# Kernel optimization log

Measured on AMD Instinct MI355X. Metric: run time of the kernel, lower is better.

## Reference

```python
import jax, jax.numpy as jnp
import numpy as np
import math

N_EMBD = 1024
N_HEAD = 16
BLOCK = 2048
SPARSITY = 0.25
B, T = 2, 2048


def _make_mask_logits(rng):
    # Replicates the patterned init in SparseMixtureAttention.__init__.
    S = BLOCK
    logits = np.empty((N_HEAD, S, S), dtype=np.float32)
    for h in range(N_HEAD):
        if h % 3 == 0:  # banded pattern (bandwidth 16)
            i = np.arange(S)
            band = (np.abs(i[:, None] - i[None, :]) <= 16)
            logits[h] = np.where(band, rng.standard_normal((S, S)) + 2.0,
                                 rng.standard_normal((S, S)) - 2.0)
        elif h % 3 == 1:  # strided pattern: every 4th column
            strided = (np.arange(S)[None, :] % 4 == 0)
            logits[h] = np.where(strided, rng.standard_normal((S, S)) + 2.0,
                                 rng.standard_normal((S, S)) - 2.0)
        else:  # random pattern with given sparsity
            rnd = rng.random((S, S)) < SPARSITY
            logits[h] = np.where(rnd, rng.standard_normal((S, S)) + 2.0,
                                 rng.standard_normal((S, S)) - 2.0)
    # keep the diagonal unmasked so no causal row is fully masked (avoids NaN rows)
    d = np.arange(S)
    logits[:, d, d] = np.abs(logits[:, d, d]) + 2.0
    return logits.astype(np.float32)


def setup_inputs() -> dict:
    key = jax.random.key(0)
    ks = jax.random.split(key, 5)
    rng = np.random.default_rng(0)
    return {
        "x": jax.random.normal(ks[0], (B, T, N_EMBD), dtype=jnp.float32),
        "mask_logits": jnp.asarray(_make_mask_logits(rng)),
        "W_attn": jax.random.normal(ks[1], (3 * N_EMBD, N_EMBD), dtype=jnp.float32) * 0.02,
        "b_attn": jnp.zeros((3 * N_EMBD,), dtype=jnp.float32),
        "W_proj": jax.random.normal(ks[2], (N_EMBD, N_EMBD), dtype=jnp.float32) * 0.02,
        "b_proj": jnp.zeros((N_EMBD,), dtype=jnp.float32),
    }


def reference(x, mask_logits, W_attn, b_attn, W_proj, b_proj):
    Bx, Tx, C = x.shape
    H = mask_logits.shape[0]
    D = C // H
    qkv = x @ W_attn.T + b_attn                       # [B,T,3C]
    q, k, v = jnp.split(qkv, 3, axis=-1)
    q = q.reshape(Bx, Tx, H, D)
    k = k.reshape(Bx, Tx, H, D)
    v = v.reshape(Bx, Tx, H, D)
    att = jnp.einsum('bthd,bshd->bhts', q, k) * (1.0 / math.sqrt(D))  # [B,H,T,T]
    # forward value of the STE mask equals the hard mask (probs - probs.detach() == 0)
    keep = jax.nn.sigmoid(mask_logits[:, :Tx, :Tx]) > 0.5             # [H,T,T]
    causal = jnp.tril(jnp.ones((Tx, Tx), dtype=bool))
    mask = causal[None, :, :] & keep                                  # [H,T,T]
    att = jnp.where(mask[None], att, -jnp.inf)
    att = jax.nn.softmax(att, axis=-1)
    y = jnp.einsum('bhts,bshd->bthd', att, v).reshape(Bx, Tx, C)
    return y @ W_proj.T + b_proj
```

## Files before the change

kernel.cpp:

```cpp
#include <hip/hip_runtime.h>
#include <hip/hip_bf16.h>
#include <stdint.h>

typedef unsigned short u16;
typedef unsigned int u32;
typedef unsigned long long u64;
typedef __attribute__((ext_vector_type(8))) short bf16x8;
typedef __attribute__((ext_vector_type(4))) float f32x4;

#define NB 2
#define NH 16
#define TT 2048
#define DD 64
#define CC 1024

__device__ __forceinline__ u16 bf16bits(float f) {
    __hip_bfloat16 h = __float2bfloat16(f);
    return __builtin_bit_cast(unsigned short, h);
}

__device__ __forceinline__ void gload_lds16(const void* g, void* l) {
    __builtin_amdgcn_global_load_lds(
        (const __attribute__((address_space(1))) void*)g,
        (__attribute__((address_space(3))) void*)l, 16, 0, 0);
}

__global__ __launch_bounds__(256) void cvt_kernel(const float* __restrict__ in,
                                                  u16* __restrict__ out, int n4) {
    int idx = blockIdx.x * blockDim.x + threadIdx.x;
    int stride = gridDim.x * blockDim.x;
    for (int i = idx; i < n4; i += stride) {
        float4 v = reinterpret_cast<const float4*>(in)[i];
        ushort4 o;
        o.x = bf16bits(v.x); o.y = bf16bits(v.y);
        o.z = bf16bits(v.z); o.w = bf16bits(v.w);
        reinterpret_cast<ushort4*>(out)[i] = o;
    }
}

__global__ __launch_bounds__(256) void mask_cvt(const float* __restrict__ ml,
                                                unsigned char* __restrict__ mb) {
    int wid = (blockIdx.x * blockDim.x + threadIdx.x) >> 6;
    int lane = threadIdx.x & 63;
    int nwaves = (gridDim.x * blockDim.x) >> 6;
    for (int row = wid; row < NH * TT; row += nwaves) {
        int i = row & (TT - 1);
        const float* src = ml + (size_t)row * TT;
        unsigned char* dst = mb + (size_t)row * (TT / 8);
        for (int c8 = lane; c8 * 8 <= i; c8 += 64) {
            const float4* p = reinterpret_cast<const float4*>(src + c8 * 8);
            float4 a = p[0];
            float4 b = p[1];
            unsigned v = 0;
            v |= (a.x > 0.f) ? 1u : 0u;
            v |= (a.y > 0.f) ? 2u : 0u;
            v |= (a.z > 0.f) ? 4u : 0u;
            v |= (a.w > 0.f) ? 8u : 0u;
            v |= (b.x > 0.f) ? 16u : 0u;
            v |= (b.y > 0.f) ? 32u : 0u;
            v |= (b.z > 0.f) ? 64u : 0u;
            v |= (b.w > 0.f) ? 128u : 0u;
            dst[c8] = (unsigned char)v;
        }
    }
}

template <int MODE>
__global__ __launch_bounds__(256) void gemm_bt(
    const u16* __restrict__ A, const u16* __restrict__ Bw,
    const float* __restrict__ bias,
    u16* __restrict__ Qb, u16* __restrict__ Kb, u16* __restrict__ Vtb,
    float* __restrict__ Cout, int Kdim) {
    const int bm = blockIdx.y * 128;
    const int bn = blockIdx.x * 128;
    const int tid = threadIdx.x;
    const int w = tid >> 6, lane = tid & 63;
    const int lrow = lane & 15, lgrp = lane >> 4;
    const int wr = (w >> 1) * 64, wc = (w & 1) * 64;

    __shared__ __align__(16) u16 ABs[2][128 * 64];
    u16* As = ABs[0];
    u16* Bs = ABs[1];

    f32x4 acc[4][4] = {};

    const int nkt = Kdim >> 6;
    for (int kt = 0; kt < nkt; ++kt) {
        const int k0 = kt << 6;
#pragma unroll
        for (int i = 0; i < 4; ++i) {
            int e = i * 2048 + tid * 8;
            int r = e >> 6, c = e & 63;
            gload_lds16(A + (size_t)(bm + r) * Kdim + k0 + c, (char*)As + i * 4096 + w * 1024);
            gload_lds16(Bw + (size_t)(bn + r) * Kdim + k0 + c, (char*)Bs + i * 4096 + w * 1024);
        }
        __syncthreads();
#pragma unroll
        for (int kk = 0; kk < 2; ++kk) {
            bf16x8 af[4], bfz[4];
#pragma unroll
            for (int i = 0; i < 4; ++i)
                af[i] = *reinterpret_cast<const bf16x8*>(&As[(wr + i * 16 + lrow) * 64 + kk * 32 + lgrp * 8]);
#pragma unroll
            for (int i = 0; i < 4; ++i)
                bfz[i] = *reinterpret_cast<const bf16x8*>(&Bs[(wc + i * 16 + lrow) * 64 + kk * 32 + lgrp * 8]);
#pragma unroll
            for (int mi = 0; mi < 4; ++mi)
#pragma unroll
                for (int ni = 0; ni < 4; ++ni)
                    acc[mi][ni] = __builtin_amdgcn_mfma_f32_16x16x32_bf16(af[mi], bfz[ni], acc[mi][ni], 0, 0, 0);
        }
        __syncthreads();
    }

    const int sec = (MODE == 0) ? (bn >> 10) : 1;

    if (MODE == 0 && sec == 2) {
        u16* Tl = &ABs[0][0];
#pragma unroll
        for (int ni = 0; ni < 4; ++ni) {
            int nl = wc + ni * 16 + lrow;
            float bv = bias[bn + nl];
#pragma unroll
            for (int mi = 0; mi < 4; ++mi) {
                int ml = wr + mi * 16 + lgrp * 4;
                u64 pk = 0;
#pragma unroll
                for (int j = 0; j < 4; ++j)
                    pk |= (u64)bf16bits(acc[mi][ni][j] + bv) << (16 * j);
                int byte = nl * 256 + ((ml * 2) ^ ((nl & 7) << 4));
                *reinterpret_cast<u64*>((char*)Tl + byte) = pk;
            }
        }
        __syncthreads();
        int r = tid >> 1, half = tid & 1;
        int h = ((bn & 1023) >> 6) + (r >> 6);
        int d = r & 63;
        int b = bm >> 11;
        u16* gdst = Vtb + (((size_t)b * NH + h) * DD + d) * TT + (bm & 2047) + half * 64;
#pragma unroll
        for (int c = 0; c < 8; ++c) {
            uint4 v = *reinterpret_cast<const uint4*>(
                (char*)Tl + r * 256 + ((half * 128 + c * 16) ^ ((r & 7) << 4)));
            *reinterpret_cast<uint4*>(gdst + c * 8) = v;
        }
        return;
    }

#pragma unroll
    for (int ni = 0; ni < 4; ++ni) {
        int n = bn + wc + ni * 16 + lrow;
        float bv = bias[n];
#pragma unroll
        for (int mi = 0; mi < 4; ++mi) {
#pragma unroll
            for (int j = 0; j < 4; ++j) {
                int m = bm + wr + mi * 16 + lgrp * 4 + j;
                float v = acc[mi][ni][j] + bv;
                if (MODE == 1) {
                    Cout[(size_t)m * 1024 + n] = v;
                } else {
                    int h = (n & 1023) >> 6;
                    int d = n & 63;
                    int b = m >> 11;
                    int t = m & 2047;
                    if (sec == 0) {
                        Qb[(((size_t)b * NH + h) * TT + t) * DD + d] =
                            bf16bits(v * (0.125f * 1.4426950408889634f));
                    } else {
                        Kb[(((size_t)b * NH + h) * TT + t) * DD + d] = bf16bits(v);
                    }
                }
            }
        }
    }
}

__global__ __launch_bounds__(256) void attn_kernel(
    const u16* __restrict__ Qb, const u16* __restrict__ Kb,
    const u16* __restrict__ Vtb, const unsigned char* __restrict__ mb,
    u16* __restrict__ att_out) {
    const int slot = blockIdx.x >> 4;
    const int h = blockIdx.x & 15;
    const int b = blockIdx.y;
    const int qt = (slot < 8) ? 31 - slot
                 : (slot < 16) ? slot + 8
                 : (slot < 24) ? 31 - slot
                 : slot - 24;
    const int tid = threadIdx.x;
    const int w = tid >> 6, lane = tid & 63;
    const int lrow = lane & 15, g = lane >> 4;

    __shared__ __align__(16) u16 Ks[2][64 * 64];
    __shared__ __align__(16) u16 Vts[2][64 * 64];
    __shared__ __align__(16) u16 Ps[4][16 * 64];

    const u16* kg_base = &Kb[((size_t)b * NH + h) * TT * DD];
    const u16* vg_base = &Vtb[((size_t)b * NH + h) * DD * TT];

    auto STAGE = [&](int bufi, int kt) {
#pragma unroll
        for (int i = 0; i < 2; ++i) {
            int e = i * 2048 + tid * 8;
            int r = e >> 6, c = e & 63;
            int cs = c ^ ((r & 7) << 3);
            gload_lds16(kg_base + (size_t)kt * 64 * DD + r * DD + cs,
                        (char*)Ks[bufi] + i * 4096 + w * 1024);
            gload_lds16(vg_base + kt * 64 + (size_t)r * TT + cs,
                        (char*)Vts[bufi] + i * 4096 + w * 1024);
        }
    };

    const int qrow_g = qt * 64 + w * 16 + lrow;
    const int rswz = (lrow & 7) << 4;

    bf16x8 qf[2];
#pragma unroll
    for (int kk = 0; kk < 2; ++kk)
        qf[kk] = *reinterpret_cast<const bf16x8*>(
            &Qb[(((size_t)b * NH + h) * TT + qrow_g) * DD + kk * 32 + g * 8]);

    f32x4 oacc[4] = {};
    float l_run = 0.f;

    const unsigned char* mrow_base = mb + ((size_t)h * TT + qrow_g) * (TT / 8);
    char* PsW = (char*)&Ps[w][0];

    STAGE(0, 0);
    __syncthreads();
    int buf = 0;

#pragma unroll 1
    for (int kt = 0; kt <= qt; ++kt) {
        u64 mw = *reinterpret_cast<const u64*>(mrow_base + kt * 8);
        if (kt < qt) STAGE(buf ^ 1, kt + 1);

        f32x4 s[4] = {};
        __builtin_amdgcn_s_setprio(1);
#pragma unroll
        for (int kk = 0; kk < 2; ++kk)
#pragma unroll
            for (int nt = 0; nt < 4; ++nt) {
                bf16x8 kf = *reinterpret_cast<const bf16x8*>(
                    (char*)Ks[buf] + (((nt * 16 + lrow) * 128 + (kk * 32 + g * 8) * 2) ^ rswz));
                s[nt] = __builtin_amdgcn_mfma_f32_16x16x32_bf16(kf, qf[kk], s[nt], 0, 0, 0);
            }
        __builtin_amdgcn_s_setprio(0);

        u64 mws = mw >> (g * 4);
        u32 mlo = (u32)mws, mhi = (u32)(mws >> 32);
        float rs = 0.f;
        if (kt == qt) {
#pragma unroll
            for (int nt = 0; nt < 4; ++nt)
#pragma unroll
                for (int j = 0; j < 4; ++j) {
                    int bi = nt * 16 + j;
                    bool keep = (((bi < 32 ? mlo : mhi) >> (bi & 31)) & 1) &&
                                (kt * 64 + nt * 16 + g * 4 + j <= qrow_g);
                    float p = keep ? exp2f(s[nt][j]) : 0.f;
                    rs += p;
                    s[nt][j] = p;
                }
        } else {
#pragma unroll
            for (int nt = 0; nt < 4; ++nt)
#pragma unroll
                for (int j = 0; j < 4; ++j) {
                    int bi = nt * 16 + j;
                    bool keep = ((bi < 32 ? mlo : mhi) >> (bi & 31)) & 1;
                    float p = keep ? exp2f(s[nt][j]) : 0.f;
                    rs += p;
                    s[nt][j] = p;
                }
        }
        rs += __shfl_xor(rs, 16);
        rs += __shfl_xor(rs, 32);
        l_run += rs;

#pragma unroll
        for (int nt = 0; nt < 4; ++nt)
#pragma unroll
            for (int t = 0; t < 2; ++t) {
                u32 pk = (u32)bf16bits(s[nt][2 * t]) |
                         ((u32)bf16bits(s[nt][2 * t + 1]) << 16);
                int byte = (lrow * 128 + (nt * 16 + g * 4 + 2 * t) * 2) ^ rswz;
                *reinterpret_cast<u32*>(PsW + byte) = pk;
            }

        __builtin_amdgcn_s_setprio(1);
#pragma unroll
        for (int kk = 0; kk < 2; ++kk) {
            bf16x8 pf = *reinterpret_cast<const bf16x8*>(
                PsW + ((lrow * 128 + (kk * 32 + g * 8) * 2) ^ rswz));
#pragma unroll
            for (int dt = 0; dt < 4; ++dt) {
                bf16x8 vf = *reinterpret_cast<const bf16x8*>(
                    (char*)Vts[buf] + (((dt * 16 + lrow) * 128 + (kk * 32 + g * 8) * 2) ^ rswz));
                oacc[dt] = __builtin_amdgcn_mfma_f32_16x16x32_bf16(pf, vf, oacc[dt], 0, 0, 0);
            }
        }
        __builtin_amdgcn_s_setprio(0);

        __syncthreads();
        buf ^= 1;
    }

    float lb[4];
#pragma unroll
    for (int j = 0; j < 4; ++j)
        lb[j] = __shfl(l_run, (lane & 48) + g * 4 + j);
#pragma unroll
    for (int dt = 0; dt < 4; ++dt)
#pragma unroll
        for (int j = 0; j < 4; ++j) {
            int t = qt * 64 + w * 16 + g * 4 + j;
            float o = oacc[dt][j] / lb[j];
            att_out[((size_t)b * TT + t) * CC + h * DD + dt * 16 + lrow] = bf16bits(o);
        }
}

extern "C" void kernel_launch(void* const* d_in, const int* in_sizes, int n_in,
                              void* d_out, int out_size, void* d_ws, size_t ws_size,
                              hipStream_t stream) {
    const float* x = (const float*)d_in[0];
    const float* mask_logits = (const float*)d_in[1];
    const float* W_attn = (const float*)d_in[2];
    const float* b_attn = (const float*)d_in[3];
    const float* W_proj = (const float*)d_in[4];
    const float* b_proj = (const float*)d_in[5];
    float* out = (float*)d_out;

    char* ws = (char*)d_ws;
    u16* xb  = (u16*)(ws + 0);
    u16* Wa  = (u16*)(ws + (8u << 20));
    u16* Wp  = (u16*)(ws + (14u << 20));
    u16* Qb  = (u16*)(ws + (16u << 20));
    u16* Kb  = (u16*)(ws + (24u << 20));
    u16* Vtb = (u16*)(ws + (32u << 20));
    u16* att = (u16*)(ws + (40u << 20));
    unsigned char* mbits = (unsigned char*)(ws + 0);

    cvt_kernel<<<2048, 256, 0, stream>>>(x, xb, NB * TT * CC / 4);
    cvt_kernel<<<2048, 256, 0, stream>>>(W_attn, Wa, 3 * CC * CC / 4);
    cvt_kernel<<<1024, 256, 0, stream>>>(W_proj, Wp, CC * CC / 4);

    gemm_bt<0><<<dim3(24, 32), 256, 0, stream>>>(xb, Wa, b_attn, Qb, Kb, Vtb, nullptr, CC);
    mask_cvt<<<1024, 256, 0, stream>>>(mask_logits, mbits);
    attn_kernel<<<dim3(512, 2), 256, 0, stream>>>(Qb, Kb, Vtb, mbits, att);
    gemm_bt<1><<<dim3(8, 32), 256, 0, stream>>>(att, Wp, b_proj, nullptr, nullptr, nullptr, out, CC);
}
```

Measured before the change: 176.4 us.

## Fuse mask bit-packing into QKV GEMM and process two query tiles per attention block

```diff
diff --git a/kernel.cpp b/kernel.cpp
--- a/kernel.cpp
+++ b/kernel.cpp
@@ -38,42 +38,44 @@
     }
 }
 
-__global__ __launch_bounds__(256) void mask_cvt(const float* __restrict__ ml,
-                                                unsigned char* __restrict__ mb) {
-    int wid = (blockIdx.x * blockDim.x + threadIdx.x) >> 6;
-    int lane = threadIdx.x & 63;
-    int nwaves = (gridDim.x * blockDim.x) >> 6;
-    for (int row = wid; row < NH * TT; row += nwaves) {
-        int i = row & (TT - 1);
-        const float* src = ml + (size_t)row * TT;
-        unsigned char* dst = mb + (size_t)row * (TT / 8);
-        for (int c8 = lane; c8 * 8 <= i; c8 += 64) {
-            const float4* p = reinterpret_cast<const float4*>(src + c8 * 8);
-            float4 a = p[0];
-            float4 b = p[1];
-            unsigned v = 0;
-            v |= (a.x > 0.f) ? 1u : 0u;
-            v |= (a.y > 0.f) ? 2u : 0u;
-            v |= (a.z > 0.f) ? 4u : 0u;
-            v |= (a.w > 0.f) ? 8u : 0u;
-            v |= (b.x > 0.f) ? 16u : 0u;
-            v |= (b.y > 0.f) ? 32u : 0u;
-            v |= (b.z > 0.f) ? 64u : 0u;
-            v |= (b.w > 0.f) ? 128u : 0u;
-            dst[c8] = (unsigned char)v;
-        }
-    }
-}
-
 template <int MODE>
 __global__ __launch_bounds__(256) void gemm_bt(
     const u16* __restrict__ A, const u16* __restrict__ Bw,
     const float* __restrict__ bias,
     u16* __restrict__ Qb, u16* __restrict__ Kb, u16* __restrict__ Vtb,
-    float* __restrict__ Cout, int Kdim) {
+    float* __restrict__ Cout, const float* __restrict__ ml,
+    unsigned char* __restrict__ mbout, int Kdim) {
+    const int tid = threadIdx.x;
+
+    if (MODE == 0 && blockIdx.x >= 24) {
+        int wid = (blockIdx.y * 8 + (blockIdx.x - 24)) * 4 + (tid >> 6);
+        int lane = tid & 63;
+#pragma unroll 1
+        for (int row = wid; row < NH * TT; row += 1024) {
+            int i = row & (TT - 1);
+            const float* src = ml + (size_t)row * TT;
+            unsigned char* dst = mbout + (size_t)row * (TT / 8);
+            for (int c8 = lane; c8 * 8 <= i; c8 += 64) {
+                const float4* p = reinterpret_cast<const float4*>(src + c8 * 8);
+                float4 a = p[0];
+                float4 bb = p[1];
+                unsigned v = 0;
+                v |= (a.x > 0.f) ? 1u : 0u;
+                v |= (a.y > 0.f) ? 2u : 0u;
+                v |= (a.z > 0.f) ? 4u : 0u;
+                v |= (a.w > 0.f) ? 8u : 0u;
+                v |= (bb.x > 0.f) ? 16u : 0u;
+                v |= (bb.y > 0.f) ? 32u : 0u;
+                v |= (bb.z > 0.f) ? 64u : 0u;
+                v |= (bb.w > 0.f) ? 128u : 0u;
+                dst[c8] = (unsigned char)v;
+            }
+        }
+        return;
+    }
+
     const int bm = blockIdx.y * 128;
     const int bn = blockIdx.x * 128;
-    const int tid = threadIdx.x;
     const int w = tid >> 6, lane = tid & 63;
     const int lrow = lane & 15, lgrp = lane >> 4;
     const int wr = (w >> 1) * 64, wc = (w & 1) * 64;
@@ -123,12 +125,12 @@
             float bv = bias[bn + nl];
 #pragma unroll
             for (int mi = 0; mi < 4; ++mi) {
-                int ml = wr + mi * 16 + lgrp * 4;
+                int ml2 = wr + mi * 16 + lgrp * 4;
                 u64 pk = 0;
 #pragma unroll
                 for (int j = 0; j < 4; ++j)
                     pk |= (u64)bf16bits(acc[mi][ni][j] + bv) << (16 * j);
-                int byte = nl * 256 + ((ml * 2) ^ ((nl & 7) << 4));
+                int byte = nl * 256 + ((ml2 * 2) ^ ((nl & 7) << 4));
                 *reinterpret_cast<u64*>((char*)Tl + byte) = pk;
             }
         }
@@ -180,20 +182,21 @@
     const u16* __restrict__ Qb, const u16* __restrict__ Kb,
     const u16* __restrict__ Vtb, const unsigned char* __restrict__ mb,
     u16* __restrict__ att_out) {
-    const int slot = blockIdx.x >> 4;
-    const int h = blockIdx.x & 15;
-    const int b = blockIdx.y;
-    const int qt = (slot < 8) ? 31 - slot
-                 : (slot < 16) ? slot + 8
-                 : (slot < 24) ? 31 - slot
-                 : slot - 24;
+    const int bid = blockIdx.x;
+    const int h = (bid >> 1) & 15;
+    const int b = bid & 1;
+    const int s8 = (bid >> 5) & 7;
+    const int qp = (bid < 256) ? (15 - s8) : s8;
+    const int t0 = 2 * qp;
+    const int nkt = t0 + 2;
+
     const int tid = threadIdx.x;
     const int w = tid >> 6, lane = tid & 63;
     const int lrow = lane & 15, g = lane >> 4;
 
     __shared__ __align__(16) u16 Ks[2][64 * 64];
     __shared__ __align__(16) u16 Vts[2][64 * 64];
-    __shared__ __align__(16) u16 Ps[4][16 * 64];
+    __shared__ __align__(16) u16 Ps[4][2][16 * 64];
 
     const u16* kg_base = &Kb[((size_t)b * NH + h) * TT * DD];
     const u16* vg_base = &Vtb[((size_t)b * NH + h) * DD * TT];
@@ -211,31 +214,40 @@
         }
     };
 
-    const int qrow_g = qt * 64 + w * 16 + lrow;
+    const int qrow0 = qp * 128 + w * 16 + lrow;
+    const int qrow1 = qrow0 + 64;
     const int rswz = (lrow & 7) << 4;
 
-    bf16x8 qf[2];
-#pragma unroll
-    for (int kk = 0; kk < 2; ++kk)
-        qf[kk] = *reinterpret_cast<const bf16x8*>(
-            &Qb[(((size_t)b * NH + h) * TT + qrow_g) * DD + kk * 32 + g * 8]);
-
-    f32x4 oacc[4] = {};
-    float l_run = 0.f;
-
-    const unsigned char* mrow_base = mb + ((size_t)h * TT + qrow_g) * (TT / 8);
-    char* PsW = (char*)&Ps[w][0];
+    bf16x8 qf0[2], qf1[2];
+#pragma unroll
+    for (int kk = 0; kk < 2; ++kk) {
+        qf0[kk] = *reinterpret_cast<const bf16x8*>(
+            &Qb[(((size_t)b * NH + h) * TT + qrow0) * DD + kk * 32 + g * 8]);
+        qf1[kk] = *reinterpret_cast<const bf16x8*>(
+            &Qb[(((size_t)b * NH + h) * TT + qrow1) * DD + kk * 32 + g * 8]);
+    }
+
+    f32x4 oacc0[4] = {}, oacc1[4] = {};
+    float l0 = 0.f, l1 = 0.f;
+
+    const unsigned char* mrow0 = mb + ((size_t)h * TT + qrow0) * (TT / 8);
+    const unsigned char* mrow1 = mrow0 + (size_t)64 * (TT / 8);
+    char* PsW0 = (char*)&Ps[w][0][0];
+    char* PsW1 = (char*)&Ps[w][1][0];
 
     STAGE(0, 0);
     __syncthreads();
     int buf = 0;
 
 #pragma unroll 1
-    for (int kt = 0; kt <= qt; ++kt) {
-        u64 mw = *reinterpret_cast<const u64*>(mrow_base + kt * 8);
-        if (kt < qt) STAGE(buf ^ 1, kt + 1);
-
-        f32x4 s[4] = {};
+    for (int kt = 0; kt < nkt; ++kt) {
+        const bool a0 = (kt <= t0);
+        u64 mw0 = 0;
+        if (a0) mw0 = *reinterpret_cast<const u64*>(mrow0 + kt * 8);
+        u64 mw1 = *reinterpret_cast<const u64*>(mrow1 + kt * 8);
+        if (kt + 1 < nkt) STAGE(buf ^ 1, kt + 1);
+
+        f32x4 s0[4] = {}, s1[4] = {};
         __builtin_amdgcn_s_setprio(1);
 #pragma unroll
         for (int kk = 0; kk < 2; ++kk)
@@ -243,61 +255,108 @@
             for (int nt = 0; nt < 4; ++nt) {
                 bf16x8 kf = *reinterpret_cast<const bf16x8*>(
                     (char*)Ks[buf] + (((nt * 16 + lrow) * 128 + (kk * 32 + g * 8) * 2) ^ rswz));
-                s[nt] = __builtin_amdgcn_mfma_f32_16x16x32_bf16(kf, qf[kk], s[nt], 0, 0, 0);
+                if (a0) s0[nt] = __builtin_amdgcn_mfma_f32_16x16x32_bf16(kf, qf0[kk], s0[nt], 0, 0, 0);
+                s1[nt] = __builtin_amdgcn_mfma_f32_16x16x32_bf16(kf, qf1[kk], s1[nt], 0, 0, 0);
             }
         __builtin_amdgcn_s_setprio(0);
 
-        u64 mws = mw >> (g * 4);
-        u32 mlo = (u32)mws, mhi = (u32)(mws >> 32);
-        float rs = 0.f;
-        if (kt == qt) {
+        if (a0) {
+            u64 mws = mw0 >> (g * 4);
+            u32 mlo = (u32)mws, mhi = (u32)(mws >> 32);
+            float rs = 0.f;
+            if (kt == t0) {
+#pragma unroll
+                for (int nt = 0; nt < 4; ++nt)
+#pragma unroll
+                    for (int j = 0; j < 4; ++j) {
+                        int bi = nt * 16 + j;
+                        bool keep = (((bi < 32 ? mlo : mhi) >> (bi & 31)) & 1) &&
+                                    (kt * 64 + nt * 16 + g * 4 + j <= qrow0);
+                        float p = keep ? exp2f(s0[nt][j]) : 0.f;
+                        rs += p;
+                        s0[nt][j] = p;
+                    }
+            } else {
+#pragma unroll
+                for (int nt = 0; nt < 4; ++nt)
+#pragma unroll
+                    for (int j = 0; j < 4; ++j) {
+                        int bi = nt * 16 + j;
+                        bool keep = ((bi < 32 ? mlo : mhi) >> (bi & 31)) & 1;
+                        float p = keep ? exp2f(s0[nt][j]) : 0.f;
+                        rs += p;
+                        s0[nt][j] = p;
+                    }
+            }
+            rs += __shfl_xor(rs, 16);
+            rs += __shfl_xor(rs, 32);
+            l0 += rs;
 #pragma unroll
             for (int nt = 0; nt < 4; ++nt)
 #pragma unroll
-                for (int j = 0; j < 4; ++j) {
-                    int bi = nt * 16 + j;
-                    bool keep = (((bi < 32 ? mlo : mhi) >> (bi & 31)) & 1) &&
-                                (kt * 64 + nt * 16 + g * 4 + j <= qrow_g);
-                    float p = keep ? exp2f(s[nt][j]) : 0.f;
-                    rs += p;
-                    s[nt][j] = p;
+                for (int t = 0; t < 2; ++t) {
+                    u32 pk = (u32)bf16bits(s0[nt][2 * t]) |
+                             ((u32)bf16bits(s0[nt][2 * t + 1]) << 16);
+                    int byte = (lrow * 128 + (nt * 16 + g * 4 + 2 * t) * 2) ^ rswz;
+                    *reinterpret_cast<u32*>(PsW0 + byte) = pk;
                 }
-        } else {
+        }
+
+        {
+            u64 mws = mw1 >> (g * 4);
+            u32 mlo = (u32)mws, mhi = (u32)(mws >> 32);
+            float rs = 0.f;
+            if (kt == t0 + 1) {
+#pragma unroll
+                for (int nt = 0; nt < 4; ++nt)
+#pragma unroll
+                    for (int j = 0; j < 4; ++j) {
+                        int bi = nt * 16 + j;
+                        bool keep = (((bi < 32 ? mlo : mhi) >> (bi & 31)) & 1) &&
+                                    (kt * 64 + nt * 16 + g * 4 + j <= qrow1);
+                        float p = keep ? exp2f(s1[nt][j]) : 0.f;
+                        rs += p;
+                        s1[nt][j] = p;
+                    }
+            } else {
+#pragma unroll
+                for (int nt = 0; nt < 4; ++nt)
+#pragma unroll
+                    for (int j = 0; j < 4; ++j) {
+                        int bi = nt * 16 + j;
+                        bool keep = ((bi < 32 ? mlo : mhi) >> (bi & 31)) & 1;
+                        float p = keep ? exp2f(s1[nt][j]) : 0.f;
+                        rs += p;
+                        s1[nt][j] = p;
+                    }
+            }
+            rs += __shfl_xor(rs, 16);
+            rs += __shfl_xor(rs, 32);
+            l1 += rs;
 #pragma unroll
             for (int nt = 0; nt < 4; ++nt)
 #pragma unroll
-                for (int j = 0; j < 4; ++j) {
-                    int bi = nt * 16 + j;
-                    bool keep = ((bi < 32 ? mlo : mhi) >> (bi & 31)) & 1;
-                    float p = keep ? exp2f(s[nt][j]) : 0.f;
-                    rs += p;
-                    s[nt][j] = p;
+                for (int t = 0; t < 2; ++t) {
+                    u32 pk = (u32)bf16bits(s1[nt][2 * t]) |
+                             ((u32)bf16bits(s1[nt][2 * t + 1]) << 16);
+                    int byte = (lrow * 128 + (nt * 16 + g * 4 + 2 * t) * 2) ^ rswz;
+                    *reinterpret_cast<u32*>(PsW1 + byte) = pk;
                 }
         }
-        rs += __shfl_xor(rs, 16);
-        rs += __shfl_xor(rs, 32);
-        l_run += rs;
-
-#pragma unroll
-        for (int nt = 0; nt < 4; ++nt)
-#pragma unroll
-            for (int t = 0; t < 2; ++t) {
-                u32 pk = (u32)bf16bits(s[nt][2 * t]) |
-                         ((u32)bf16bits(s[nt][2 * t + 1]) << 16);
-                int byte = (lrow * 128 + (nt * 16 + g * 4 + 2 * t) * 2) ^ rswz;
-                *reinterpret_cast<u32*>(PsW + byte) = pk;
-            }
 
         __builtin_amdgcn_s_setprio(1);
 #pragma unroll
         for (int kk = 0; kk < 2; ++kk) {
-            bf16x8 pf = *reinterpret_cast<const bf16x8*>(
-                PsW + ((lrow * 128 + (kk * 32 + g * 8) * 2) ^ rswz));
+            int pb = (lrow * 128 + (kk * 32 + g * 8) * 2) ^ rswz;
+            bf16x8 pf0;
+            if (a0) pf0 = *reinterpret_cast<const bf16x8*>(PsW0 + pb);
+            bf16x8 pf1 = *reinterpret_cast<const bf16x8*>(PsW1 + pb);
 #pragma unroll
             for (int dt = 0; dt < 4; ++dt) {
                 bf16x8 vf = *reinterpret_cast<const bf16x8*>(
                     (char*)Vts[buf] + (((dt * 16 + lrow) * 128 + (kk * 32 + g * 8) * 2) ^ rswz));
-                oacc[dt] = __builtin_amdgcn_mfma_f32_16x16x32_bf16(pf, vf, oacc[dt], 0, 0, 0);
+                if (a0) oacc0[dt] = __builtin_amdgcn_mfma_f32_16x16x32_bf16(pf0, vf, oacc0[dt], 0, 0, 0);
+                oacc1[dt] = __builtin_amdgcn_mfma_f32_16x16x32_bf16(pf1, vf, oacc1[dt], 0, 0, 0);
             }
         }
         __builtin_amdgcn_s_setprio(0);
@@ -306,17 +365,21 @@
         buf ^= 1;
     }
 
-    float lb[4];
-#pragma unroll
-    for (int j = 0; j < 4; ++j)
-        lb[j] = __shfl(l_run, (lane & 48) + g * 4 + j);
+    float lb0[4], lb1[4];
+#pragma unroll
+    for (int j = 0; j < 4; ++j) {
+        lb0[j] = __shfl(l0, (lane & 48) + g * 4 + j);
+        lb1[j] = __shfl(l1, (lane & 48) + g * 4 + j);
+    }
 #pragma unroll
     for (int dt = 0; dt < 4; ++dt)
 #pragma unroll
         for (int j = 0; j < 4; ++j) {
-            int t = qt * 64 + w * 16 + g * 4 + j;
-            float o = oacc[dt][j] / lb[j];
-            att_out[((size_t)b * TT + t) * CC + h * DD + dt * 16 + lrow] = bf16bits(o);
+            int t = qp * 128 + w * 16 + g * 4 + j;
+            float o0 = oacc0[dt][j] / lb0[j];
+            float o1 = oacc1[dt][j] / lb1[j];
+            att_out[((size_t)b * TT + t) * CC + h * DD + dt * 16 + lrow] = bf16bits(o0);
+            att_out[((size_t)b * TT + t + 64) * CC + h * DD + dt * 16 + lrow] = bf16bits(o1);
         }
 }
 
@@ -339,14 +402,15 @@
     u16* Kb  = (u16*)(ws + (24u << 20));
     u16* Vtb = (u16*)(ws + (32u << 20));
     u16* att = (u16*)(ws + (40u << 20));
-    unsigned char* mbits = (unsigned char*)(ws + 0);
+    unsigned char* mbits = (unsigned char*)(ws + (48u << 20));
 
     cvt_kernel<<<2048, 256, 0, stream>>>(x, xb, NB * TT * CC / 4);
     cvt_kernel<<<2048, 256, 0, stream>>>(W_attn, Wa, 3 * CC * CC / 4);
     cvt_kernel<<<1024, 256, 0, stream>>>(W_proj, Wp, CC * CC / 4);
 
-    gemm_bt<0><<<dim3(24, 32), 256, 0, stream>>>(xb, Wa, b_attn, Qb, Kb, Vtb, nullptr, CC);
-    mask_cvt<<<1024, 256, 0, stream>>>(mask_logits, mbits);
-    attn_kernel<<<dim3(512, 2), 256, 0, stream>>>(Qb, Kb, Vtb, mbits, att);
-    gemm_bt<1><<<dim3(8, 32), 256, 0, stream>>>(att, Wp, b_proj, nullptr, nullptr, nullptr, out, CC);
-}
+    gemm_bt<0><<<dim3(32, 32), 256, 0, stream>>>(xb, Wa, b_attn, Qb, Kb, Vtb,
+                                                 nullptr, mask_logits, mbits, CC);
+    attn_kernel<<<512, 256, 0, stream>>>(Qb, Kb, Vtb, mbits, att);
+    gemm_bt<1><<<dim3(8, 32), 256, 0, stream>>>(att, Wp, b_proj, nullptr, nullptr, nullptr,
+                                                out, nullptr, nullptr, CC);
+}
```

After: 220.5 us. 1.25x slower.

## Fuse mask bit-packing into QKV GEMM launch as extra blocks

Applied to the files above, without the earlier changes.

```diff
diff --git a/kernel.cpp b/kernel.cpp
--- a/kernel.cpp
+++ b/kernel.cpp
@@ -38,42 +38,44 @@
     }
 }
 
-__global__ __launch_bounds__(256) void mask_cvt(const float* __restrict__ ml,
-                                                unsigned char* __restrict__ mb) {
-    int wid = (blockIdx.x * blockDim.x + threadIdx.x) >> 6;
-    int lane = threadIdx.x & 63;
-    int nwaves = (gridDim.x * blockDim.x) >> 6;
-    for (int row = wid; row < NH * TT; row += nwaves) {
-        int i = row & (TT - 1);
-        const float* src = ml + (size_t)row * TT;
-        unsigned char* dst = mb + (size_t)row * (TT / 8);
-        for (int c8 = lane; c8 * 8 <= i; c8 += 64) {
-            const float4* p = reinterpret_cast<const float4*>(src + c8 * 8);
-            float4 a = p[0];
-            float4 b = p[1];
-            unsigned v = 0;
-            v |= (a.x > 0.f) ? 1u : 0u;
-            v |= (a.y > 0.f) ? 2u : 0u;
-            v |= (a.z > 0.f) ? 4u : 0u;
-            v |= (a.w > 0.f) ? 8u : 0u;
-            v |= (b.x > 0.f) ? 16u : 0u;
-            v |= (b.y > 0.f) ? 32u : 0u;
-            v |= (b.z > 0.f) ? 64u : 0u;
-            v |= (b.w > 0.f) ? 128u : 0u;
-            dst[c8] = (unsigned char)v;
-        }
-    }
-}
-
 template <int MODE>
 __global__ __launch_bounds__(256) void gemm_bt(
     const u16* __restrict__ A, const u16* __restrict__ Bw,
     const float* __restrict__ bias,
     u16* __restrict__ Qb, u16* __restrict__ Kb, u16* __restrict__ Vtb,
-    float* __restrict__ Cout, int Kdim) {
+    float* __restrict__ Cout, const float* __restrict__ ml,
+    unsigned char* __restrict__ mbout, int Kdim) {
+    const int tid = threadIdx.x;
+
+    if (MODE == 0 && blockIdx.x >= 24) {
+        int wid = (blockIdx.y * 8 + (blockIdx.x - 24)) * 4 + (tid >> 6);
+        int lane = tid & 63;
+#pragma unroll 1
+        for (int row = wid; row < NH * TT; row += 1024) {
+            int i = row & (TT - 1);
+            const float* src = ml + (size_t)row * TT;
+            unsigned char* dst = mbout + (size_t)row * (TT / 8);
+            for (int c8 = lane; c8 * 8 <= i; c8 += 64) {
+                const float4* p = reinterpret_cast<const float4*>(src + c8 * 8);
+                float4 a = p[0];
+                float4 bb = p[1];
+                unsigned v = 0;
+                v |= (a.x > 0.f) ? 1u : 0u;
+                v |= (a.y > 0.f) ? 2u : 0u;
+                v |= (a.z > 0.f) ? 4u : 0u;
+                v |= (a.w > 0.f) ? 8u : 0u;
+                v |= (bb.x > 0.f) ? 16u : 0u;
+                v |= (bb.y > 0.f) ? 32u : 0u;
+                v |= (bb.z > 0.f) ? 64u : 0u;
+                v |= (bb.w > 0.f) ? 128u : 0u;
+                dst[c8] = (unsigned char)v;
+            }
+        }
+        return;
+    }
+
     const int bm = blockIdx.y * 128;
     const int bn = blockIdx.x * 128;
-    const int tid = threadIdx.x;
     const int w = tid >> 6, lane = tid & 63;
     const int lrow = lane & 15, lgrp = lane >> 4;
     const int wr = (w >> 1) * 64, wc = (w & 1) * 64;
@@ -123,12 +125,12 @@
             float bv = bias[bn + nl];
 #pragma unroll
             for (int mi = 0; mi < 4; ++mi) {
-                int ml = wr + mi * 16 + lgrp * 4;
+                int ml2 = wr + mi * 16 + lgrp * 4;
                 u64 pk = 0;
 #pragma unroll
                 for (int j = 0; j < 4; ++j)
                     pk |= (u64)bf16bits(acc[mi][ni][j] + bv) << (16 * j);
-                int byte = nl * 256 + ((ml * 2) ^ ((nl & 7) << 4));
+                int byte = nl * 256 + ((ml2 * 2) ^ ((nl & 7) << 4));
                 *reinterpret_cast<u64*>((char*)Tl + byte) = pk;
             }
         }
@@ -339,14 +341,15 @@
     u16* Kb  = (u16*)(ws + (24u << 20));
     u16* Vtb = (u16*)(ws + (32u << 20));
     u16* att = (u16*)(ws + (40u << 20));
-    unsigned char* mbits = (unsigned char*)(ws + 0);
+    unsigned char* mbits = (unsigned char*)(ws + (48u << 20));
 
     cvt_kernel<<<2048, 256, 0, stream>>>(x, xb, NB * TT * CC / 4);
     cvt_kernel<<<2048, 256, 0, stream>>>(W_attn, Wa, 3 * CC * CC / 4);
     cvt_kernel<<<1024, 256, 0, stream>>>(W_proj, Wp, CC * CC / 4);
 
-    gemm_bt<0><<<dim3(24, 32), 256, 0, stream>>>(xb, Wa, b_attn, Qb, Kb, Vtb, nullptr, CC);
-    mask_cvt<<<1024, 256, 0, stream>>>(mask_logits, mbits);
+    gemm_bt<0><<<dim3(32, 32), 256, 0, stream>>>(xb, Wa, b_attn, Qb, Kb, Vtb,
+                                                 nullptr, mask_logits, mbits, CC);
     attn_kernel<<<dim3(512, 2), 256, 0, stream>>>(Qb, Kb, Vtb, mbits, att);
-    gemm_bt<1><<<dim3(8, 32), 256, 0, stream>>>(att, Wp, b_proj, nullptr, nullptr, nullptr, out, CC);
-}
+    gemm_bt<1><<<dim3(8, 32), 256, 0, stream>>>(att, Wp, b_proj, nullptr, nullptr, nullptr,
+                                                out, nullptr, nullptr, CC);
+}
```

Measured after the change: 200.2 us. +13.5%, slower.
